# Kernel optimization log

Measured on AMD Instinct MI355X. Metric: run time of the kernel, lower is better.

## Reference

```python
import jax, jax.numpy as jnp
import numpy as np

N_HEADS = 16
HEAD_DIM = 64  # dim=1024 / n_heads=16


def setup_inputs() -> dict:
    key = jax.random.key(0)
    ks = jax.random.split(key, 7)
    B, S, D = 4, 2048, 1024
    scale = 1.0 / np.sqrt(D)
    return {
        "q": jax.random.normal(ks[0], (B, S, D), jnp.float32),
        "k": jax.random.normal(ks[1], (B, S, D), jnp.float32),
        "v": jax.random.normal(ks[2], (B, S, D), jnp.float32),
        "Wq": jax.random.normal(ks[3], (D, D), jnp.float32) * scale,
        "Wk": jax.random.normal(ks[4], (D, D), jnp.float32) * scale,
        "Wv": jax.random.normal(ks[5], (D, D), jnp.float32) * scale,
        "Wo": jax.random.normal(ks[6], (D, D), jnp.float32) * scale,
    }


def reference(q, k, v, Wq, Wk, Wv, Wo):
    B, S, _ = q.shape
    H, Dh = N_HEADS, HEAD_DIM
    # linear projections (torch Linear: x @ W.T), reshape to [B, H, S, Dh]
    xq = (q @ Wq.T).reshape(B, S, H, Dh).transpose(0, 2, 1, 3)
    xk = (k @ Wk.T).reshape(B, S, H, Dh).transpose(0, 2, 1, 3)
    xv = (v @ Wv.T).reshape(B, S, H, Dh).transpose(0, 2, 1, 3)
    scores = jnp.einsum("bhsd,bhtd->bhst", xq, xk) / jnp.sqrt(jnp.float32(Dh))
    # causal mask: -inf above diagonal
    causal = jnp.triu(jnp.full((S, S), -jnp.inf, jnp.float32), k=1)
    scores = scores + causal[None, None]
    attn = jax.nn.softmax(scores.astype(jnp.float32), axis=-1).astype(xq.dtype)
    out = jnp.einsum("bhst,bhtd->bhsd", attn, xv)
    out = out.transpose(0, 2, 1, 3).reshape(B, S, H * Dh)
    return out @ Wo.T
```

## Files before the change

### kernel.cpp

```cpp
#include <hip/hip_runtime.h>
#include <hip/hip_bf16.h>

#define DI __device__ __forceinline__

typedef __attribute__((ext_vector_type(8))) short short8;
typedef __attribute__((ext_vector_type(4))) short short4v;
typedef __attribute__((ext_vector_type(4))) float f32x4;

DI short f2bf(float f) {
  unsigned u = __builtin_bit_cast(unsigned, f);
  unsigned r = u + 0x7fffu + ((u >> 16) & 1u);
  return (short)(r >> 16);
}

DI void gl16(const short* g, short* l) {
  __builtin_amdgcn_global_load_lds(
      (const __attribute__((address_space(1))) void*)g,
      (__attribute__((address_space(3))) void*)l, 16, 0, 0);
}

__global__ __launch_bounds__(256) void convert_w(
    const float* __restrict__ wq, const float* __restrict__ wk,
    const float* __restrict__ wv, const float* __restrict__ wo,
    short* __restrict__ dst) {
  int z = blockIdx.z;
  const float* src = (z == 0) ? wq : (z == 1) ? wk : (z == 2) ? wv : wo;
  short* d = dst + (size_t)z * 1024 * 1024;
  int i = (blockIdx.x * 256 + threadIdx.x) * 4;
  float4 f = *(const float4*)(src + i);
  short4v v;
  v[0] = f2bf(f.x); v[1] = f2bf(f.y); v[2] = f2bf(f.z); v[3] = f2bf(f.w);
  *(short4v*)(d + i) = v;
}

__global__ __launch_bounds__(256) void convert_x(
    const float* __restrict__ q, const float* __restrict__ k,
    const float* __restrict__ v, short* __restrict__ qb,
    short* __restrict__ kb, short* __restrict__ vb) {
  int z = blockIdx.z;
  const float* src = (z == 0) ? q : (z == 1) ? k : v;
  short* dst = (z == 0) ? qb : (z == 1) ? kb : vb;
  size_t i = ((size_t)blockIdx.x * 256 + threadIdx.x) * 8;
  float4 f0 = *(const float4*)(src + i);
  float4 f1 = *(const float4*)(src + i + 4);
  short8 o;
  o[0] = f2bf(f0.x); o[1] = f2bf(f0.y); o[2] = f2bf(f0.z); o[3] = f2bf(f0.w);
  o[4] = f2bf(f1.x); o[5] = f2bf(f1.y); o[6] = f2bf(f1.z); o[7] = f2bf(f1.w);
  *(short8*)(dst + i) = o;
}

__global__ __launch_bounds__(256) void convert_one(
    const float* __restrict__ src, short* __restrict__ dst) {
  size_t i = ((size_t)blockIdx.x * 256 + threadIdx.x) * 8;
  float4 f0 = *(const float4*)(src + i);
  float4 f1 = *(const float4*)(src + i + 4);
  short8 o;
  o[0] = f2bf(f0.x); o[1] = f2bf(f0.y); o[2] = f2bf(f0.z); o[3] = f2bf(f0.w);
  o[4] = f2bf(f1.x); o[5] = f2bf(f1.y); o[6] = f2bf(f1.z); o[7] = f2bf(f1.w);
  *(short8*)(dst + i) = o;
}

template <bool OUT_HEAD>
DI void gemm_core(const short* __restrict__ A, const short* __restrict__ B,
                  void* __restrict__ Cp, float scale, int bm, int bn) {
  __shared__ __align__(16) short sA[128 * 64];
  __shared__ __align__(16) short sB[128 * 64];

  const int tid = threadIdx.x;
  const int lane = tid & 63;
  const int wid = tid >> 6;
  const int wm = wid >> 1, wn = wid & 1;
  const int l15 = lane & 15, lq = lane >> 4;
  const int lrr = lane >> 3;
  const int lch = lane & 7;

  f32x4 acc[4][4] = {};

  for (int k0 = 0; k0 < 1024; k0 += 64) {
#pragma unroll
    for (int i = 0; i < 4; ++i) {
      int r0 = wid * 32 + i * 8;
      int rr = r0 + lrr;
      int sc = (lch ^ (rr & 7)) << 3;
      gl16(A + (size_t)(bm + rr) * 1024 + k0 + sc, sA + r0 * 64);
      gl16(B + (size_t)(bn + rr) * 1024 + k0 + sc, sB + r0 * 64);
    }
    __syncthreads();

#pragma unroll
    for (int ks = 0; ks < 2; ++ks) {
      short8 a[4], b[4];
#pragma unroll
      for (int mt = 0; mt < 4; ++mt) {
        int row = wm * 64 + mt * 16 + l15;
        int off = (row * 128 + ks * 64 + lq * 16) ^ ((row & 7) << 4);
        a[mt] = *(const short8*)((const char*)sA + off);
      }
#pragma unroll
      for (int nt = 0; nt < 4; ++nt) {
        int row = wn * 64 + nt * 16 + l15;
        int off = (row * 128 + ks * 64 + lq * 16) ^ ((row & 7) << 4);
        b[nt] = *(const short8*)((const char*)sB + off);
      }
#pragma unroll
      for (int mt = 0; mt < 4; ++mt)
#pragma unroll
        for (int nt = 0; nt < 4; ++nt)
          acc[mt][nt] = __builtin_amdgcn_mfma_f32_16x16x32_bf16(
              a[mt], b[nt], acc[mt][nt], 0, 0, 0);
    }
    __syncthreads();
  }

#pragma unroll
  for (int mt = 0; mt < 4; ++mt) {
#pragma unroll
    for (int nt = 0; nt < 4; ++nt) {
#pragma unroll
      for (int r = 0; r < 4; ++r) {
        int rowg = bm + wm * 64 + mt * 16 + lq * 4 + r;
        int colg = bn + wn * 64 + nt * 16 + l15;
        float val = acc[mt][nt][r] * scale;
        if (OUT_HEAD) {
          int b = rowg >> 11, s = rowg & 2047;
          int h = colg >> 6, dh = colg & 63;
          ((short*)Cp)[((size_t)(b * 16 + h) * 2048 + s) * 64 + dh] = f2bf(val);
        } else {
          ((float*)Cp)[(size_t)rowg * 1024 + colg] = val;
        }
      }
    }
  }
}

DI void xcd_map(int id, int& bm, int& bn) {
  int xcd = id & 7, slot = id >> 3;
  int panel = xcd + 8 * (slot >> 3);
  int ntile = slot & 7;
  bm = panel * 128;
  bn = ntile * 128;
}

__global__ __launch_bounds__(256) void proj_gemm3(
    const short* __restrict__ qb, const short* __restrict__ kb,
    const short* __restrict__ vb, const short* __restrict__ wq,
    const short* __restrict__ wk, const short* __restrict__ wv,
    short* __restrict__ xq, short* __restrict__ xk, short* __restrict__ xv) {
  int z = blockIdx.z;
  const short* A = (z == 0) ? qb : (z == 1) ? kb : vb;
  const short* B = (z == 0) ? wq : (z == 1) ? wk : wv;
  short* C = (z == 0) ? xq : (z == 1) ? xk : xv;
  float scale = (z == 0) ? 0.125f : 1.0f;
  int bm, bn;
  xcd_map(blockIdx.x, bm, bn);
  gemm_core<true>(A, B, C, scale, bm, bn);
}

__global__ __launch_bounds__(256) void proj_one(
    const short* __restrict__ A, const short* __restrict__ B,
    short* __restrict__ C, float scale) {
  int bm, bn;
  xcd_map(blockIdx.x, bm, bn);
  gemm_core<true>(A, B, C, scale, bm, bn);
}

__global__ __launch_bounds__(256) void final_gemm(
    const short* __restrict__ oa, const short* __restrict__ wo,
    float* __restrict__ out) {
  int bm, bn;
  xcd_map(blockIdx.x, bm, bn);
  gemm_core<false>(oa, wo, out, 1.0f, bm, bn);
}

__global__ __launch_bounds__(256) void transpose_v(
    const short* __restrict__ Xv, short* __restrict__ XvT) {
  __shared__ __align__(16) short sT[64 * 64];
  const int tid = threadIdx.x;
  const int bh = blockIdx.y;
  const int s0 = blockIdx.x * 64;
  const short* src = Xv + ((size_t)bh * 2048 + s0) * 64;
  short* dst = XvT + (size_t)bh * 64 * 2048 + s0;
#pragma unroll
  for (int t = 0; t < 2; ++t) {
    int c = tid + t * 256;
    int r = c >> 3, c8 = (c & 7) * 8;
    short8 v = *(const short8*)(src + (size_t)r * 64 + c8);
    int off = (r * 128 + c8 * 2) ^ (((r ^ (r >> 3)) & 7) << 4);
    *(short8*)((char*)sT + off) = v;
  }
  __syncthreads();
#pragma unroll
  for (int u = 0; u < 2; ++u) {
    int c = tid + u * 256;
    int dh = c >> 3;
    int sl = (c & 7) * 8;
    short8 o;
#pragma unroll
    for (int i = 0; i < 8; ++i) {
      int r = sl + i;
      int off = (r * 128 + dh * 2) ^ (((r ^ (r >> 3)) & 7) << 4);
      o[i] = *(const short*)((const char*)sT + off);
    }
    *(short8*)(dst + (size_t)dh * 2048 + sl) = o;
  }
}

__global__ __launch_bounds__(256) void attn_k(
    const short* __restrict__ Xq, const short* __restrict__ Xk,
    const short* __restrict__ XvT, short* __restrict__ Oa) {
  __shared__ __align__(16) short sK[64 * 64];
  __shared__ __align__(16) short sVT[64 * 64];
  __shared__ __align__(16) short sP[4][16 * 64];

  const int tid = threadIdx.x;
  const int lane = tid & 63;
  const int wid = tid >> 6;
  const int l15 = lane & 15, lq = lane >> 4;
  const int bid = blockIdx.x;
  const int ipair = bid >> 6;
  const int bh = bid & 63;
  const int b = bh >> 4, h = bh & 15;

  const short* Q = Xq + (size_t)bh * 2048 * 64;
  const short* K = Xk + (size_t)bh * 2048 * 64;
  const short* VT = XvT + (size_t)bh * 64 * 2048;

  const int srow = tid >> 3;
  const int scol = (tid & 7) * 8;
  const int soff0 = (srow * 128 + scol * 2) ^ ((srow & 7) << 4);
  const int soff1 = ((srow + 32) * 128 + scol * 2) ^ ((srow & 7) << 4);

  short8 kreg[2], vreg[2];
  kreg[0] = *(const short8*)(K + (size_t)srow * 64 + scol);
  kreg[1] = *(const short8*)(K + (size_t)(srow + 32) * 64 + scol);
  vreg[0] = *(const short8*)(VT + (size_t)srow * 2048 + scol);
  vreg[1] = *(const short8*)(VT + (size_t)(srow + 32) * 2048 + scol);

  short* sPw = sP[wid];

  for (int seg = 0; seg < 2; ++seg) {
    const int qt = seg ? ipair : (31 - ipair);
    const int qrow0 = qt * 64 + wid * 16;
    const int qg = qrow0 + l15;

    short8 qf[2];
#pragma unroll
    for (int ks = 0; ks < 2; ++ks)
      qf[ks] = *(const short8*)(Q + (size_t)qg * 64 + ks * 32 + lq * 8);

    float m_run = -1e30f, l_run = 0.f;
    f32x4 acc[4] = {};

    for (int kt = 0; kt <= qt; ++kt) {
      const int kv0 = kt * 64;
      *(short8*)((char*)sK + soff0) = kreg[0];
      *(short8*)((char*)sK + soff1) = kreg[1];
      *(short8*)((char*)sVT + soff0) = vreg[0];
      *(short8*)((char*)sVT + soff1) = vreg[1];
      __syncthreads();

      {
        int nkt = kt + 1, nseg = seg;
        if (nkt > qt) { nseg = seg + 1; nkt = 0; }
        if (nseg < 2) {
          const int kn = nkt * 64;
          kreg[0] = *(const short8*)(K + (size_t)(kn + srow) * 64 + scol);
          kreg[1] = *(const short8*)(K + (size_t)(kn + srow + 32) * 64 + scol);
          vreg[0] = *(const short8*)(VT + (size_t)srow * 2048 + kn + scol);
          vreg[1] = *(const short8*)(VT + (size_t)(srow + 32) * 2048 + kn + scol);
        }
      }

      f32x4 sc[4] = {};
      __builtin_amdgcn_s_setprio(1);
#pragma unroll
      for (int ks = 0; ks < 2; ++ks) {
        short8 kf[4];
#pragma unroll
        for (int nt = 0; nt < 4; ++nt) {
          int row = nt * 16 + l15;
          int off = (row * 128 + ks * 64 + lq * 16) ^ ((row & 7) << 4);
          kf[nt] = *(const short8*)((const char*)sK + off);
        }
#pragma unroll
        for (int nt = 0; nt < 4; ++nt)
          sc[nt] = __builtin_amdgcn_mfma_f32_16x16x32_bf16(kf[nt], qf[ks], sc[nt], 0, 0, 0);
      }
      __builtin_amdgcn_s_setprio(0);

      float p[4][4];
      float m = -1e30f;
      const bool diag = (kt == qt);
#pragma unroll
      for (int nt = 0; nt < 4; ++nt) {
#pragma unroll
        for (int r = 0; r < 4; ++r) {
          float s = sc[nt][r];
          if (diag && (kv0 + nt * 16 + lq * 4 + r > qg)) s = -1e30f;
          p[nt][r] = s;
          m = fmaxf(m, s);
        }
      }
      m = fmaxf(m, __shfl_xor(m, 16));
      m = fmaxf(m, __shfl_xor(m, 32));

      const float m_new = fmaxf(m_run, m);
      const float corr = __expf(m_run - m_new);
      float rsum = 0.f;
#pragma unroll
      for (int nt = 0; nt < 4; ++nt)
#pragma unroll
        for (int r = 0; r < 4; ++r) {
          float e = __expf(p[nt][r] - m_new);
          p[nt][r] = e;
          rsum += e;
        }
      rsum += __shfl_xor(rsum, 16);
      rsum += __shfl_xor(rsum, 32);
      l_run = l_run * corr + rsum;
      m_run = m_new;
#pragma unroll
      for (int mt = 0; mt < 4; ++mt)
#pragma unroll
        for (int r = 0; r < 4; ++r) acc[mt][r] *= corr;

#pragma unroll
      for (int nt = 0; nt < 4; ++nt) {
        short4v pw;
#pragma unroll
        for (int r = 0; r < 4; ++r) pw[r] = f2bf(p[nt][r]);
        int off = (l15 * 128 + nt * 32 + lq * 8) ^ ((l15 & 7) << 4);
        *(short4v*)((char*)sPw + off) = pw;
      }

      __builtin_amdgcn_s_setprio(1);
#pragma unroll
      for (int ks = 0; ks < 2; ++ks) {
        int poff = (l15 * 128 + ks * 64 + lq * 16) ^ ((l15 & 7) << 4);
        short8 pf = *(const short8*)((const char*)sPw + poff);
#pragma unroll
        for (int mt = 0; mt < 4; ++mt) {
          int row = mt * 16 + l15;
          int voff = (row * 128 + ks * 64 + lq * 16) ^ ((row & 7) << 4);
          short8 vf = *(const short8*)((const char*)sVT + voff);
          acc[mt] = __builtin_amdgcn_mfma_f32_16x16x32_bf16(vf, pf, acc[mt], 0, 0, 0);
        }
      }
      __builtin_amdgcn_s_setprio(0);
      __syncthreads();
    }

    const float rl = 1.0f / l_run;
    short* orow = Oa + ((size_t)(b * 2048 + qg)) * 1024 + h * 64;
#pragma unroll
    for (int mt = 0; mt < 4; ++mt) {
      short4v o;
#pragma unroll
      for (int r = 0; r < 4; ++r) o[r] = f2bf(acc[mt][r] * rl);
      *(short4v*)(orow + mt * 16 + lq * 4) = o;
    }
  }
}

extern "C" void kernel_launch(void* const* d_in, const int* in_sizes, int n_in,
                              void* d_out, int out_size, void* d_ws,
                              size_t ws_size, hipStream_t stream) {
  const float* q = (const float*)d_in[0];
  const float* k = (const float*)d_in[1];
  const float* v = (const float*)d_in[2];
  const float* Wq = (const float*)d_in[3];
  const float* Wk = (const float*)d_in[4];
  const float* Wv = (const float*)d_in[5];
  const float* Wo = (const float*)d_in[6];

  char* ws = (char*)d_ws;
  short* wq_b = (short*)(ws + (0ull << 20));
  short* wk_b = (short*)(ws + (2ull << 20));
  short* wv_b = (short*)(ws + (4ull << 20));
  short* wo_b = (short*)(ws + (6ull << 20));
  short* xq  = (short*)(ws + (8ull << 20));
  short* xk  = (short*)(ws + (24ull << 20));
  short* xv  = (short*)(ws + (40ull << 20));
  short* xvT = (short*)(ws + (56ull << 20));

  convert_w<<<dim3(1024, 1, 4), 256, 0, stream>>>(Wq, Wk, Wv, Wo, wq_b);

  if (ws_size >= (122ull << 20)) {
    short* qb = (short*)(ws + (72ull << 20));
    short* kb = (short*)(ws + (88ull << 20));
    short* vb = (short*)(ws + (104ull << 20));
    short* oa = qb;

    convert_x<<<dim3(4096, 1, 3), 256, 0, stream>>>(q, k, v, qb, kb, vb);
    proj_gemm3<<<dim3(512, 1, 3), 256, 0, stream>>>(qb, kb, vb, wq_b, wk_b,
                                                    wv_b, xq, xk, xv);
    transpose_v<<<dim3(32, 64), 256, 0, stream>>>(xv, xvT);
    attn_k<<<dim3(1024), 256, 0, stream>>>(xq, xk, xvT, oa);
    final_gemm<<<dim3(512), 256, 0, stream>>>(oa, wo_b, (float*)d_out);
  } else {
    short* X = (short*)(ws + (8ull << 20));
    short* xq2 = (short*)(ws + (24ull << 20));
    short* xk2 = (short*)(ws + (40ull << 20));
    short* xv2 = (short*)(ws + (56ull << 20));
    short* xvT2 = (short*)(ws + (72ull << 20));

    convert_one<<<dim3(4096), 256, 0, stream>>>(q, X);
    proj_one<<<dim3(512), 256, 0, stream>>>(X, wq_b, xq2, 0.125f);
    convert_one<<<dim3(4096), 256, 0, stream>>>(k, X);
    proj_one<<<dim3(512), 256, 0, stream>>>(X, wk_b, xk2, 1.0f);
    convert_one<<<dim3(4096), 256, 0, stream>>>(v, X);
    proj_one<<<dim3(512), 256, 0, stream>>>(X, wv_b, xv2, 1.0f);
    transpose_v<<<dim3(32, 64), 256, 0, stream>>>(xv2, xvT2);
    attn_k<<<dim3(1024), 256, 0, stream>>>(xq2, xk2, xvT2, X);
    final_gemm<<<dim3(512), 256, 0, stream>>>(X, wo_b, (float*)d_out);
  }
}
```

Measured before the change: 200.4 us.

## Fuse V transpose into projection epilogue, use exp2 softmax with lazy rescale

Folds log2(e) into the Q projection scale so softmax uses exp2, and skips the running-max rescale unless the max grows by more than 8 (in log2 units). Writes V directly in transposed head layout from the projection GEMM by swapping MFMA operands, which removes the separate transpose kernel and its extra memory round trip. Packs bf16 conversions with the v_cvt_pk_bf16_f32 instruction. The transposed epilogue writes along s with a stride-2048 pattern, which may be less coalesced, and lazy rescaling lets unnormalised values grow up to 2^8.

```diff
diff --git a/kernel.cpp b/kernel.cpp
--- a/kernel.cpp
+++ b/kernel.cpp
@@ -6,11 +6,27 @@
 typedef __attribute__((ext_vector_type(8))) short short8;
 typedef __attribute__((ext_vector_type(4))) short short4v;
 typedef __attribute__((ext_vector_type(4))) float f32x4;
+
+#define QSCALE 0.180336885f
 
 DI short f2bf(float f) {
   unsigned u = __builtin_bit_cast(unsigned, f);
   unsigned r = u + 0x7fffu + ((u >> 16) & 1u);
   return (short)(r >> 16);
+}
+
+DI unsigned cvt_pk(float lo, float hi) {
+  unsigned r;
+  asm("v_cvt_pk_bf16_f32 %0, %1, %2" : "=v"(r) : "v"(lo), "v"(hi));
+  return r;
+}
+
+DI float fexp2(float x) {
+#if __has_builtin(__builtin_amdgcn_exp2f)
+  return __builtin_amdgcn_exp2f(x);
+#else
+  return exp2f(x);
+#endif
 }
 
 DI void gl16(const short* g, short* l) {
@@ -60,7 +76,9 @@
   *(short8*)(dst + i) = o;
 }
 
-template <bool OUT_HEAD>
+enum { OUT_F32 = 0, OUT_HEAD = 1, OUT_HEADT = 2 };
+
+template <int OMODE>
 DI void gemm_core(const short* __restrict__ A, const short* __restrict__ B,
                   void* __restrict__ Cp, float scale, int bm, int bn) {
   __shared__ __align__(16) short sA[128 * 64];
@@ -105,9 +123,14 @@
 #pragma unroll
       for (int mt = 0; mt < 4; ++mt)
 #pragma unroll
-        for (int nt = 0; nt < 4; ++nt)
-          acc[mt][nt] = __builtin_amdgcn_mfma_f32_16x16x32_bf16(
-              a[mt], b[nt], acc[mt][nt], 0, 0, 0);
+        for (int nt = 0; nt < 4; ++nt) {
+          if (OMODE == OUT_HEADT)
+            acc[mt][nt] = __builtin_amdgcn_mfma_f32_16x16x32_bf16(
+                b[nt], a[mt], acc[mt][nt], 0, 0, 0);
+          else
+            acc[mt][nt] = __builtin_amdgcn_mfma_f32_16x16x32_bf16(
+                a[mt], b[nt], acc[mt][nt], 0, 0, 0);
+        }
     }
     __syncthreads();
   }
@@ -118,15 +141,23 @@
     for (int nt = 0; nt < 4; ++nt) {
 #pragma unroll
       for (int r = 0; r < 4; ++r) {
-        int rowg = bm + wm * 64 + mt * 16 + lq * 4 + r;
-        int colg = bn + wn * 64 + nt * 16 + l15;
         float val = acc[mt][nt][r] * scale;
-        if (OUT_HEAD) {
-          int b = rowg >> 11, s = rowg & 2047;
-          int h = colg >> 6, dh = colg & 63;
-          ((short*)Cp)[((size_t)(b * 16 + h) * 2048 + s) * 64 + dh] = f2bf(val);
+        if (OMODE == OUT_HEADT) {
+          int f = bn + wn * 64 + nt * 16 + lq * 4 + r;
+          int t = bm + wm * 64 + mt * 16 + l15;
+          int bb = t >> 11, s = t & 2047;
+          int h = f >> 6, dh = f & 63;
+          ((short*)Cp)[((size_t)((bb * 16 + h) * 64 + dh)) * 2048 + s] = f2bf(val);
         } else {
-          ((float*)Cp)[(size_t)rowg * 1024 + colg] = val;
+          int rowg = bm + wm * 64 + mt * 16 + lq * 4 + r;
+          int colg = bn + wn * 64 + nt * 16 + l15;
+          if (OMODE == OUT_HEAD) {
+            int bb = rowg >> 11, s = rowg & 2047;
+            int h = colg >> 6, dh = colg & 63;
+            ((short*)Cp)[((size_t)(bb * 16 + h) * 2048 + s) * 64 + dh] = f2bf(val);
+          } else {
+            ((float*)Cp)[(size_t)rowg * 1024 + colg] = val;
+          }
         }
       }
     }
@@ -145,23 +176,33 @@
     const short* __restrict__ qb, const short* __restrict__ kb,
     const short* __restrict__ vb, const short* __restrict__ wq,
     const short* __restrict__ wk, const short* __restrict__ wv,
-    short* __restrict__ xq, short* __restrict__ xk, short* __restrict__ xv) {
+    short* __restrict__ xq, short* __restrict__ xk, short* __restrict__ xvT) {
   int z = blockIdx.z;
-  const short* A = (z == 0) ? qb : (z == 1) ? kb : vb;
-  const short* B = (z == 0) ? wq : (z == 1) ? wk : wv;
-  short* C = (z == 0) ? xq : (z == 1) ? xk : xv;
-  float scale = (z == 0) ? 0.125f : 1.0f;
   int bm, bn;
   xcd_map(blockIdx.x, bm, bn);
-  gemm_core<true>(A, B, C, scale, bm, bn);
-}
-
-__global__ __launch_bounds__(256) void proj_one(
+  if (z == 0) {
+    gemm_core<OUT_HEAD>(qb, wq, xq, QSCALE, bm, bn);
+  } else if (z == 1) {
+    gemm_core<OUT_HEAD>(kb, wk, xk, 1.0f, bm, bn);
+  } else {
+    gemm_core<OUT_HEADT>(vb, wv, xvT, 1.0f, bm, bn);
+  }
+}
+
+__global__ __launch_bounds__(256) void proj_oneN(
     const short* __restrict__ A, const short* __restrict__ B,
     short* __restrict__ C, float scale) {
   int bm, bn;
   xcd_map(blockIdx.x, bm, bn);
-  gemm_core<true>(A, B, C, scale, bm, bn);
+  gemm_core<OUT_HEAD>(A, B, C, scale, bm, bn);
+}
+
+__global__ __launch_bounds__(256) void proj_oneT(
+    const short* __restrict__ A, const short* __restrict__ B,
+    short* __restrict__ C, float scale) {
+  int bm, bn;
+  xcd_map(blockIdx.x, bm, bn);
+  gemm_core<OUT_HEADT>(A, B, C, scale, bm, bn);
 }
 
 __global__ __launch_bounds__(256) void final_gemm(
@@ -169,40 +210,7 @@
     float* __restrict__ out) {
   int bm, bn;
   xcd_map(blockIdx.x, bm, bn);
-  gemm_core<false>(oa, wo, out, 1.0f, bm, bn);
-}
-
-__global__ __launch_bounds__(256) void transpose_v(
-    const short* __restrict__ Xv, short* __restrict__ XvT) {
-  __shared__ __align__(16) short sT[64 * 64];
-  const int tid = threadIdx.x;
-  const int bh = blockIdx.y;
-  const int s0 = blockIdx.x * 64;
-  const short* src = Xv + ((size_t)bh * 2048 + s0) * 64;
-  short* dst = XvT + (size_t)bh * 64 * 2048 + s0;
-#pragma unroll
-  for (int t = 0; t < 2; ++t) {
-    int c = tid + t * 256;
-    int r = c >> 3, c8 = (c & 7) * 8;
-    short8 v = *(const short8*)(src + (size_t)r * 64 + c8);
-    int off = (r * 128 + c8 * 2) ^ (((r ^ (r >> 3)) & 7) << 4);
-    *(short8*)((char*)sT + off) = v;
-  }
-  __syncthreads();
-#pragma unroll
-  for (int u = 0; u < 2; ++u) {
-    int c = tid + u * 256;
-    int dh = c >> 3;
-    int sl = (c & 7) * 8;
-    short8 o;
-#pragma unroll
-    for (int i = 0; i < 8; ++i) {
-      int r = sl + i;
-      int off = (r * 128 + dh * 2) ^ (((r ^ (r >> 3)) & 7) << 4);
-      o[i] = *(const short*)((const char*)sT + off);
-    }
-    *(short8*)(dst + (size_t)dh * 2048 + sl) = o;
-  }
+  gemm_core<OUT_F32>(oa, wo, out, 1.0f, bm, bn);
 }
 
 __global__ __launch_bounds__(256) void attn_k(
@@ -304,33 +312,37 @@
       m = fmaxf(m, __shfl_xor(m, 16));
       m = fmaxf(m, __shfl_xor(m, 32));
 
-      const float m_new = fmaxf(m_run, m);
-      const float corr = __expf(m_run - m_new);
+      if (!__all(m - m_run <= 8.0f)) {
+        const float m_new = fmaxf(m_run, m);
+        const float corr = fexp2(m_run - m_new);
+        l_run *= corr;
+#pragma unroll
+        for (int mt = 0; mt < 4; ++mt)
+#pragma unroll
+          for (int r = 0; r < 4; ++r) acc[mt][r] *= corr;
+        m_run = m_new;
+      }
+
       float rsum = 0.f;
 #pragma unroll
       for (int nt = 0; nt < 4; ++nt)
 #pragma unroll
         for (int r = 0; r < 4; ++r) {
-          float e = __expf(p[nt][r] - m_new);
+          float e = fexp2(p[nt][r] - m_run);
           p[nt][r] = e;
           rsum += e;
         }
       rsum += __shfl_xor(rsum, 16);
       rsum += __shfl_xor(rsum, 32);
-      l_run = l_run * corr + rsum;
-      m_run = m_new;
-#pragma unroll
-      for (int mt = 0; mt < 4; ++mt)
-#pragma unroll
-        for (int r = 0; r < 4; ++r) acc[mt][r] *= corr;
+      l_run += rsum;
 
 #pragma unroll
       for (int nt = 0; nt < 4; ++nt) {
-        short4v pw;
-#pragma unroll
-        for (int r = 0; r < 4; ++r) pw[r] = f2bf(p[nt][r]);
+        uint2 pw;
+        pw.x = cvt_pk(p[nt][0], p[nt][1]);
+        pw.y = cvt_pk(p[nt][2], p[nt][3]);
         int off = (l15 * 128 + nt * 32 + lq * 8) ^ ((l15 & 7) << 4);
-        *(short4v*)((char*)sPw + off) = pw;
+        *(uint2*)((char*)sPw + off) = pw;
       }
 
       __builtin_amdgcn_s_setprio(1);
@@ -354,10 +366,10 @@
     short* orow = Oa + ((size_t)(b * 2048 + qg)) * 1024 + h * 64;
 #pragma unroll
     for (int mt = 0; mt < 4; ++mt) {
-      short4v o;
-#pragma unroll
-      for (int r = 0; r < 4; ++r) o[r] = f2bf(acc[mt][r] * rl);
-      *(short4v*)(orow + mt * 16 + lq * 4) = o;
+      uint2 o;
+      o.x = cvt_pk(acc[mt][0] * rl, acc[mt][1] * rl);
+      o.y = cvt_pk(acc[mt][2] * rl, acc[mt][3] * rl);
+      *(uint2*)(orow + mt * 16 + lq * 4) = o;
     }
   }
 }
@@ -380,7 +392,6 @@
   short* wo_b = (short*)(ws + (6ull << 20));
   short* xq  = (short*)(ws + (8ull << 20));
   short* xk  = (short*)(ws + (24ull << 20));
-  short* xv  = (short*)(ws + (40ull << 20));
   short* xvT = (short*)(ws + (56ull << 20));
 
   convert_w<<<dim3(1024, 1, 4), 256, 0, stream>>>(Wq, Wk, Wv, Wo, wq_b);
@@ -393,25 +404,23 @@
 
     convert_x<<<dim3(4096, 1, 3), 256, 0, stream>>>(q, k, v, qb, kb, vb);
     proj_gemm3<<<dim3(512, 1, 3), 256, 0, stream>>>(qb, kb, vb, wq_b, wk_b,
-                                                    wv_b, xq, xk, xv);
-    transpose_v<<<dim3(32, 64), 256, 0, stream>>>(xv, xvT);
+                                                    wv_b, xq, xk, xvT);
     attn_k<<<dim3(1024), 256, 0, stream>>>(xq, xk, xvT, oa);
     final_gemm<<<dim3(512), 256, 0, stream>>>(oa, wo_b, (float*)d_out);
   } else {
     short* X = (short*)(ws + (8ull << 20));
     short* xq2 = (short*)(ws + (24ull << 20));
     short* xk2 = (short*)(ws + (40ull << 20));
-    short* xv2 = (short*)(ws + (56ull << 20));
-    short* xvT2 = (short*)(ws + (72ull << 20));
+    short* xvT2 = (short*)(ws + (56ull << 20));
+    short* oa2 = (short*)(ws + (72ull << 20));
 
     convert_one<<<dim3(4096), 256, 0, stream>>>(q, X);
-    proj_one<<<dim3(512), 256, 0, stream>>>(X, wq_b, xq2, 0.125f);
+    proj_oneN<<<dim3(512), 256, 0, stream>>>(X, wq_b, xq2, QSCALE);
     convert_one<<<dim3(4096), 256, 0, stream>>>(k, X);
-    proj_one<<<dim3(512), 256, 0, stream>>>(X, wk_b, xk2, 1.0f);
+    proj_oneN<<<dim3(512), 256, 0, stream>>>(X, wk_b, xk2, 1.0f);
     convert_one<<<dim3(4096), 256, 0, stream>>>(v, X);
-    proj_one<<<dim3(512), 256, 0, stream>>>(X, wv_b, xv2, 1.0f);
-    transpose_v<<<dim3(32, 64), 256, 0, stream>>>(xv2, xvT2);
-    attn_k<<<dim3(1024), 256, 0, stream>>>(xq2, xk2, xvT2, X);
-    final_gemm<<<dim3(512), 256, 0, stream>>>(X, wo_b, (float*)d_out);
+    proj_oneT<<<dim3(512), 256, 0, stream>>>(X, wv_b, xvT2, 1.0f);
+    attn_k<<<dim3(1024), 256, 0, stream>>>(xq2, xk2, xvT2, oa2);
+    final_gemm<<<dim3(512), 256, 0, stream>>>(oa2, wo_b, (float*)d_out);
   }
 }
```

Result: no change. 197.8 us (-1.3%).
